# Kernel optimization log

Measured on AMD Instinct MI355X. Metric: run time of the kernel, lower is better.

## Reference

```python
import jax, jax.numpy as jnp
import numpy as np

WINDOW = 2048
STRIDE = 512
FREQ = WINDOW // 2  # 1024
FRAMES = 63
SIG_LEN = FRAMES * STRIDE  # 32256
BATCH = 64


def _make_kernels():
    # Hann window, sym=False: w[n] = 0.5*(1 - cos(2*pi*n/N))
    n = np.arange(WINDOW)
    window = 0.5 * (1.0 - np.cos(2.0 * np.pi * n / WINDOW))
    f = np.arange(FREQ)
    # basis[f, n] = exp(-2j*pi*f*n/N) * window[n]  (first N/2 rows of windowed DFT)
    phase = -2.0 * np.pi * np.outer(f, n) / WINDOW
    real = (np.cos(phase) * window[None, :]).T[:, None, :]  # [W, 1, F]
    imag = (np.sin(phase) * window[None, :]).T[:, None, :]  # [W, 1, F]
    return jnp.asarray(real, jnp.float32), jnp.asarray(imag, jnp.float32)


def setup_inputs() -> dict:
    key = jax.random.key(0)
    input_signal = jax.random.normal(key, (BATCH, SIG_LEN, 1), dtype=jnp.float32)
    real_kernel, imag_kernel = _make_kernels()
    return {"input_signal": input_signal, "real_kernel": real_kernel, "imag_kernel": imag_kernel}


def _stft(x, k):
    # TF 'same' padding for stride 512, kernel 2048, out = ceil(L/512) = 63:
    # total_pad = (out-1)*stride + kernel - L = 62*512 + 2048 - 32256 = 1536
    pad_l, pad_r = 768, 768
    return jax.lax.conv_general_dilated(
        x, k, window_strides=(STRIDE,), padding=[(pad_l, pad_r)],
        dimension_numbers=("NWC", "WIO", "NWC"))  # [B, 63, 1024]


def reference(input_signal, real_kernel, imag_kernel):
    real = _stft(input_signal, real_kernel)
    imag = _stft(input_signal, imag_kernel)
    real = real.reshape(-1, FRAMES, FREQ, 1)
    imag = imag.reshape(-1, FRAMES, FREQ, 1)
    return real, imag
```

## Files before the change

### kernel.cpp

```cpp
#include <hip/hip_runtime.h>
#include <hip/hip_bf16.h>

#define WINDOW   2048
#define STRIDE   512
#define FREQ     1024
#define FRAMES   63
#define SIG_LEN  32256
#define BATCH    64
#define PAD      768
#define XPAD_LEN 33792
#define M_TOTAL  4032
#define N_TOTAL  2048
#define K_TOTAL  2048

#define BM 128
#define BN 128
#define BK 64

typedef __attribute__((ext_vector_type(8))) short short8;
typedef __attribute__((ext_vector_type(4))) float floatx4;

__device__ __forceinline__ ushort f2bf(float f) {
    __hip_bfloat16 h = __float2bfloat16(f);
    return *reinterpret_cast<ushort*>(&h);
}

__global__ void pad_signal(const float4* __restrict__ x, uint4* __restrict__ xpad) {
    int id = blockIdx.x * blockDim.x + threadIdx.x;
    const int GP = XPAD_LEN / 8;
    if (id >= BATCH * GP) return;
    int b = id / GP, i = id - b * GP;
    ushort o[8] = {0, 0, 0, 0, 0, 0, 0, 0};
    int s = i - PAD / 8;
    if (s >= 0 && s < SIG_LEN / 8) {
        const float4* px = x + (size_t)b * (SIG_LEN / 4) + s * 2;
        float4 v0 = px[0], v1 = px[1];
        o[0] = f2bf(v0.x); o[1] = f2bf(v0.y); o[2] = f2bf(v0.z); o[3] = f2bf(v0.w);
        o[4] = f2bf(v1.x); o[5] = f2bf(v1.y); o[6] = f2bf(v1.z); o[7] = f2bf(v1.w);
    }
    xpad[id] = *(uint4*)o;
}

__global__ void build_bt(const float* __restrict__ kr,
                         const float* __restrict__ ki,
                         ushort* __restrict__ bt) {
    __shared__ __align__(16) ushort tile[64][72];
    const int tid = threadIdx.x;
    const int kt = blockIdx.x, nt = blockIdx.y;
    const int gn0 = nt * 64;
    const float* src = (gn0 < FREQ) ? kr : ki;
    const int n0 = gn0 - ((gn0 < FREQ) ? 0 : FREQ);
#pragma unroll
    for (int i = 0; i < 2; ++i) {
        int chunk = i * 256 + tid;
        int k = chunk >> 3, nc = chunk & 7;
        const float* p = src + (size_t)(kt * 64 + k) * FREQ + n0 + nc * 8;
        float4 v0 = *(const float4*)p;
        float4 v1 = *(const float4*)(p + 4);
        ushort tmp[8];
        tmp[0] = f2bf(v0.x); tmp[1] = f2bf(v0.y); tmp[2] = f2bf(v0.z); tmp[3] = f2bf(v0.w);
        tmp[4] = f2bf(v1.x); tmp[5] = f2bf(v1.y); tmp[6] = f2bf(v1.z); tmp[7] = f2bf(v1.w);
        *(uint4*)(&tile[k][nc * 8]) = *(uint4*)tmp;
    }
    __syncthreads();
#pragma unroll
    for (int i = 0; i < 2; ++i) {
        int chunk = i * 256 + tid;
        int n = chunk >> 3, kc = chunk & 7;
        ushort tmp[8];
#pragma unroll
        for (int j = 0; j < 8; ++j) tmp[j] = tile[kc * 8 + j][n];
        *(uint4*)(bt + (size_t)(gn0 + n) * K_TOTAL + kt * 64 + kc * 8) = *(uint4*)tmp;
    }
}

__device__ __forceinline__ void gload16(const ushort* g, ushort* l) {
    __builtin_amdgcn_global_load_lds(
        (const __attribute__((address_space(1))) unsigned int*)g,
        (__attribute__((address_space(3))) unsigned int*)l,
        16, 0, 0);
}

__global__ __launch_bounds__(256) void stft_gemm(
    const ushort* __restrict__ xpad, const ushort* __restrict__ bt,
    float* __restrict__ out) {
    __shared__ __align__(16) ushort As[2 * BM * 32];
    __shared__ __align__(16) ushort Bs[2 * BN * 32];

    const int tid  = threadIdx.x;
    const int lane = tid & 63;
    const int w    = tid >> 6;
    const int mtile = blockIdx.x;
    const int ntile = blockIdx.y;

    const int srow = w * 16 + (lane >> 2);
    const int kcol = ((lane & 3) ^ ((lane >> 3) & 3)) * 8;

    int gr0 = mtile * BM + srow;
    int gr1 = gr0 + 64;
    gr0 = min(gr0, M_TOTAL - 1);
    gr1 = min(gr1, M_TOTAL - 1);
    const int b0 = gr0 / FRAMES, t0 = gr0 - b0 * FRAMES;
    const int b1 = gr1 / FRAMES, t1 = gr1 - b1 * FRAMES;
    const ushort* gA0 = xpad + (size_t)b0 * XPAD_LEN + t0 * STRIDE + kcol;
    const ushort* gA1 = xpad + (size_t)b1 * XPAD_LEN + t1 * STRIDE + kcol;
    const ushort* gB0 = bt + (size_t)(ntile * BN + srow) * K_TOTAL + kcol;
    const ushort* gB1 = gB0 + (size_t)64 * K_TOTAL;

    ushort* ldsA0 = As + w * 512;
    ushort* ldsA1 = As + 2048 + w * 512;
    ushort* ldsB0 = Bs + w * 512;
    ushort* ldsB1 = Bs + 2048 + w * 512;

    const int wm = w >> 1, wn = w & 1;
    const int frow = lane & 15, fq = lane >> 4;
    const int cs = (fq ^ ((frow >> 1) & 3)) * 8;
    const ushort* pA = As + (wm * 64 + frow) * 32 + cs;
    const ushort* pB = Bs + (wn * 64 + frow) * 32 + cs;

    floatx4 acc[4][4];
#pragma unroll
    for (int mi = 0; mi < 4; ++mi)
#pragma unroll
        for (int ni = 0; ni < 4; ++ni)
            acc[mi][ni] = (floatx4){0.f, 0.f, 0.f, 0.f};

    for (int kt = 0; kt < K_TOTAL / BK; ++kt) {
        __syncthreads();
        gload16(gA0,      ldsA0);
        gload16(gA0 + 32, ldsA0 + 4096);
        gload16(gA1,      ldsA1);
        gload16(gA1 + 32, ldsA1 + 4096);
        gload16(gB0,      ldsB0);
        gload16(gB0 + 32, ldsB0 + 4096);
        gload16(gB1,      ldsB1);
        gload16(gB1 + 32, ldsB1 + 4096);
        gA0 += BK; gA1 += BK; gB0 += BK; gB1 += BK;
        __syncthreads();

#pragma unroll
        for (int kk = 0; kk < 2; ++kk) {
            short8 a[4], b[4];
#pragma unroll
            for (int mi = 0; mi < 4; ++mi)
                a[mi] = *(const short8*)(pA + kk * 4096 + mi * 512);
#pragma unroll
            for (int ni = 0; ni < 4; ++ni)
                b[ni] = *(const short8*)(pB + kk * 4096 + ni * 512);
#pragma unroll
            for (int mi = 0; mi < 4; ++mi)
#pragma unroll
                for (int ni = 0; ni < 4; ++ni)
                    acc[mi][ni] = __builtin_amdgcn_mfma_f32_16x16x32_bf16(
                        a[mi], b[ni], acc[mi][ni], 0, 0, 0);
        }
    }

    const int orow0 = mtile * BM + wm * 64 + fq * 4;
    const bool is_imag = (ntile >= 8);
    float* outp = out + (is_imag ? (size_t)M_TOTAL * FREQ : 0);
    const int ncol0 = (ntile - (is_imag ? 8 : 0)) * BN + wn * 64 + frow;

#pragma unroll
    for (int mi = 0; mi < 4; ++mi) {
#pragma unroll
        for (int r = 0; r < 4; ++r) {
            int grow = orow0 + mi * 16 + r;
            if (grow < M_TOTAL) {
                float* orow = outp + (size_t)grow * FREQ + ncol0;
#pragma unroll
                for (int ni = 0; ni < 4; ++ni)
                    orow[ni * 16] = acc[mi][ni][r];
            }
        }
    }
}

extern "C" void kernel_launch(void* const* d_in, const int* in_sizes, int n_in,
                              void* d_out, int out_size, void* d_ws, size_t ws_size,
                              hipStream_t stream) {
    const float* x  = (const float*)d_in[0];
    const float* kr = (const float*)d_in[1];
    const float* ki = (const float*)d_in[2];

    ushort* xpad = (ushort*)d_ws;
    ushort* btm  = xpad + (size_t)BATCH * XPAD_LEN;

    pad_signal<<<(BATCH * XPAD_LEN / 8 + 255) / 256, 256, 0, stream>>>(
        (const float4*)x, (uint4*)xpad);
    build_bt<<<dim3(K_TOTAL / 64, N_TOTAL / 64), 256, 0, stream>>>(kr, ki, btm);
    stft_gemm<<<dim3((M_TOTAL + BM - 1) / BM, N_TOTAL / BN), 256, 0, stream>>>(
        xpad, btm, (float*)d_out);
}
```

Measured before the change: 118.6 us.

## Register-prefetch next K tile instead of direct global-to-LDS loads

Replaces the global_load_lds direct copies with ordinary global loads into registers that are issued for the next K tile while the current tile's MFMAs run. The registers are then stored to LDS at the top of the next iteration. This is meant to hide global memory latency behind compute, since the previous loop waited on each load before computing. The cost is more VGPR pressure and extra LDS store instructions, and occupancy may drop as a result.

New measurement: 122.3 us. +3.1%, slower.

```diff
diff --git a/kernel.cpp b/kernel.cpp
--- a/kernel.cpp
+++ b/kernel.cpp
@@ -74,13 +74,6 @@
     }
 }
 
-__device__ __forceinline__ void gload16(const ushort* g, ushort* l) {
-    __builtin_amdgcn_global_load_lds(
-        (const __attribute__((address_space(1))) unsigned int*)g,
-        (__attribute__((address_space(3))) unsigned int*)l,
-        16, 0, 0);
-}
-
 __global__ __launch_bounds__(256) void stft_gemm(
     const ushort* __restrict__ xpad, const ushort* __restrict__ bt,
     float* __restrict__ out) {
@@ -107,10 +100,14 @@
     const ushort* gB0 = bt + (size_t)(ntile * BN + srow) * K_TOTAL + kcol;
     const ushort* gB1 = gB0 + (size_t)64 * K_TOTAL;
 
-    ushort* ldsA0 = As + w * 512;
-    ushort* ldsA1 = As + 2048 + w * 512;
-    ushort* ldsB0 = Bs + w * 512;
-    ushort* ldsB1 = Bs + 2048 + w * 512;
+    uint4* sA0 = (uint4*)(As + w * 512) + lane;
+    uint4* sA0h = (uint4*)(As + w * 512 + 4096) + lane;
+    uint4* sA1 = (uint4*)(As + 2048 + w * 512) + lane;
+    uint4* sA1h = (uint4*)(As + 2048 + w * 512 + 4096) + lane;
+    uint4* sB0 = (uint4*)(Bs + w * 512) + lane;
+    uint4* sB0h = (uint4*)(Bs + w * 512 + 4096) + lane;
+    uint4* sB1 = (uint4*)(Bs + 2048 + w * 512) + lane;
+    uint4* sB1h = (uint4*)(Bs + 2048 + w * 512 + 4096) + lane;
 
     const int wm = w >> 1, wn = w & 1;
     const int frow = lane & 15, fq = lane >> 4;
@@ -125,35 +122,52 @@
         for (int ni = 0; ni < 4; ++ni)
             acc[mi][ni] = (floatx4){0.f, 0.f, 0.f, 0.f};
 
+    uint4 va0, va0h, va1, va1h, vb0, vb0h, vb1, vb1h;
+    va0  = *(const uint4*)gA0;  va0h = *(const uint4*)(gA0 + 32);
+    va1  = *(const uint4*)gA1;  va1h = *(const uint4*)(gA1 + 32);
+    vb0  = *(const uint4*)gB0;  vb0h = *(const uint4*)(gB0 + 32);
+    vb1  = *(const uint4*)gB1;  vb1h = *(const uint4*)(gB1 + 32);
+    gA0 += BK; gA1 += BK; gB0 += BK; gB1 += BK;
+
     for (int kt = 0; kt < K_TOTAL / BK; ++kt) {
         __syncthreads();
-        gload16(gA0,      ldsA0);
-        gload16(gA0 + 32, ldsA0 + 4096);
-        gload16(gA1,      ldsA1);
-        gload16(gA1 + 32, ldsA1 + 4096);
-        gload16(gB0,      ldsB0);
-        gload16(gB0 + 32, ldsB0 + 4096);
-        gload16(gB1,      ldsB1);
-        gload16(gB1 + 32, ldsB1 + 4096);
-        gA0 += BK; gA1 += BK; gB0 += BK; gB1 += BK;
+        *sA0 = va0;  *sA0h = va0h;
+        *sA1 = va1;  *sA1h = va1h;
+        *sB0 = vb0;  *sB0h = vb0h;
+        *sB1 = vb1;  *sB1h = vb1h;
         __syncthreads();
 
-#pragma unroll
-        for (int kk = 0; kk < 2; ++kk) {
-            short8 a[4], b[4];
-#pragma unroll
-            for (int mi = 0; mi < 4; ++mi)
-                a[mi] = *(const short8*)(pA + kk * 4096 + mi * 512);
+        short8 a[4], b[4];
+#pragma unroll
+        for (int mi = 0; mi < 4; ++mi) a[mi] = *(const short8*)(pA + mi * 512);
+#pragma unroll
+        for (int ni = 0; ni < 4; ++ni) b[ni] = *(const short8*)(pB + ni * 512);
+
+        if (kt < K_TOTAL / BK - 1) {
+            va0  = *(const uint4*)gA0;  va0h = *(const uint4*)(gA0 + 32);
+            va1  = *(const uint4*)gA1;  va1h = *(const uint4*)(gA1 + 32);
+            vb0  = *(const uint4*)gB0;  vb0h = *(const uint4*)(gB0 + 32);
+            vb1  = *(const uint4*)gB1;  vb1h = *(const uint4*)(gB1 + 32);
+            gA0 += BK; gA1 += BK; gB0 += BK; gB1 += BK;
+        }
+
+#pragma unroll
+        for (int mi = 0; mi < 4; ++mi)
 #pragma unroll
             for (int ni = 0; ni < 4; ++ni)
-                b[ni] = *(const short8*)(pB + kk * 4096 + ni * 512);
-#pragma unroll
-            for (int mi = 0; mi < 4; ++mi)
-#pragma unroll
-                for (int ni = 0; ni < 4; ++ni)
-                    acc[mi][ni] = __builtin_amdgcn_mfma_f32_16x16x32_bf16(
-                        a[mi], b[ni], acc[mi][ni], 0, 0, 0);
-        }
+                acc[mi][ni] = __builtin_amdgcn_mfma_f32_16x16x32_bf16(
+                    a[mi], b[ni], acc[mi][ni], 0, 0, 0);
+
+#pragma unroll
+        for (int mi = 0; mi < 4; ++mi) a[mi] = *(const short8*)(pA + 4096 + mi * 512);
+#pragma unroll
+        for (int ni = 0; ni < 4; ++ni) b[ni] = *(const short8*)(pB + 4096 + ni * 512);
+#pragma unroll
+        for (int mi = 0; mi < 4; ++mi)
+#pragma unroll
+            for (int ni = 0; ni < 4; ++ni)
+                acc[mi][ni] = __builtin_amdgcn_mfma_f32_16x16x32_bf16(
+                    a[mi], b[ni], acc[mi][ni], 0, 0, 0);
     }
 
     const int orow0 = mtile * BM + wm * 64 + fq * 4;
```

## Switch GEMM to 32x32x16 MFMA and fuse the prep kernels into one launch

Applied to the files above, without the earlier changes.

The GEMM inner loop now uses 32x32x16 bf16 MFMA tiles, two by two per wave, in place of sixteen 16x16x32 tiles, with new LDS addressing and output index mapping. This cuts LDS fragment reads per MFMA and the number of MFMA issues. Separately, the pad and basis-transpose kernels are merged into one launch, with a block-index split, to save one kernel launch. The new swizzle and lane mapping must line up with the existing store layout or results will be wrong.

New measurement: 116.0 us. -2.2%, faster.

```diff
diff --git a/kernel.cpp b/kernel.cpp
--- a/kernel.cpp
+++ b/kernel.cpp
@@ -17,60 +17,63 @@
 #define BN 128
 #define BK 64
 
-typedef __attribute__((ext_vector_type(8))) short short8;
-typedef __attribute__((ext_vector_type(4))) float floatx4;
+#define PAD_BLOCKS 1056
+
+typedef __attribute__((ext_vector_type(8)))  short short8;
+typedef __attribute__((ext_vector_type(16))) float floatx16;
 
 __device__ __forceinline__ ushort f2bf(float f) {
     __hip_bfloat16 h = __float2bfloat16(f);
     return *reinterpret_cast<ushort*>(&h);
 }
 
-__global__ void pad_signal(const float4* __restrict__ x, uint4* __restrict__ xpad) {
-    int id = blockIdx.x * blockDim.x + threadIdx.x;
-    const int GP = XPAD_LEN / 8;
-    if (id >= BATCH * GP) return;
-    int b = id / GP, i = id - b * GP;
-    ushort o[8] = {0, 0, 0, 0, 0, 0, 0, 0};
-    int s = i - PAD / 8;
-    if (s >= 0 && s < SIG_LEN / 8) {
-        const float4* px = x + (size_t)b * (SIG_LEN / 4) + s * 2;
-        float4 v0 = px[0], v1 = px[1];
-        o[0] = f2bf(v0.x); o[1] = f2bf(v0.y); o[2] = f2bf(v0.z); o[3] = f2bf(v0.w);
-        o[4] = f2bf(v1.x); o[5] = f2bf(v1.y); o[6] = f2bf(v1.z); o[7] = f2bf(v1.w);
-    }
-    xpad[id] = *(uint4*)o;
-}
-
-__global__ void build_bt(const float* __restrict__ kr,
-                         const float* __restrict__ ki,
-                         ushort* __restrict__ bt) {
-    __shared__ __align__(16) ushort tile[64][72];
+__global__ __launch_bounds__(256) void prep_fused(
+    const float* __restrict__ x, const float* __restrict__ kr,
+    const float* __restrict__ ki, ushort* __restrict__ xpad_o,
+    ushort* __restrict__ bt) {
     const int tid = threadIdx.x;
-    const int kt = blockIdx.x, nt = blockIdx.y;
-    const int gn0 = nt * 64;
-    const float* src = (gn0 < FREQ) ? kr : ki;
-    const int n0 = gn0 - ((gn0 < FREQ) ? 0 : FREQ);
+    if (blockIdx.x < PAD_BLOCKS) {
+        int id = blockIdx.x * 256 + tid;
+        const int GP = XPAD_LEN / 8;
+        int b = id / GP, i = id - b * GP;
+        ushort o[8] = {0, 0, 0, 0, 0, 0, 0, 0};
+        int s = i - PAD / 8;
+        if (s >= 0 && s < SIG_LEN / 8) {
+            const float4* px = (const float4*)x + (size_t)b * (SIG_LEN / 4) + s * 2;
+            float4 v0 = px[0], v1 = px[1];
+            o[0] = f2bf(v0.x); o[1] = f2bf(v0.y); o[2] = f2bf(v0.z); o[3] = f2bf(v0.w);
+            o[4] = f2bf(v1.x); o[5] = f2bf(v1.y); o[6] = f2bf(v1.z); o[7] = f2bf(v1.w);
+        }
+        ((uint4*)xpad_o)[id] = *(uint4*)o;
+    } else {
+        __shared__ __align__(16) ushort tile[64][72];
+        const int bid = blockIdx.x - PAD_BLOCKS;
+        const int kt = bid & 31, nt = bid >> 5;
+        const int gn0 = nt * 64;
+        const float* src = (gn0 < FREQ) ? kr : ki;
+        const int n0 = gn0 - ((gn0 < FREQ) ? 0 : FREQ);
 #pragma unroll
-    for (int i = 0; i < 2; ++i) {
-        int chunk = i * 256 + tid;
-        int k = chunk >> 3, nc = chunk & 7;
-        const float* p = src + (size_t)(kt * 64 + k) * FREQ + n0 + nc * 8;
-        float4 v0 = *(const float4*)p;
-        float4 v1 = *(const float4*)(p + 4);
-        ushort tmp[8];
-        tmp[0] = f2bf(v0.x); tmp[1] = f2bf(v0.y); tmp[2] = f2bf(v0.z); tmp[3] = f2bf(v0.w);
-        tmp[4] = f2bf(v1.x); tmp[5] = f2bf(v1.y); tmp[6] = f2bf(v1.z); tmp[7] = f2bf(v1.w);
-        *(uint4*)(&tile[k][nc * 8]) = *(uint4*)tmp;
-    }
-    __syncthreads();
+        for (int i = 0; i < 2; ++i) {
+            int chunk = i * 256 + tid;
+            int k = chunk >> 3, nc = chunk & 7;
+            const float* p = src + (size_t)(kt * 64 + k) * FREQ + n0 + nc * 8;
+            float4 v0 = *(const float4*)p;
+            float4 v1 = *(const float4*)(p + 4);
+            ushort tmp[8];
+            tmp[0] = f2bf(v0.x); tmp[1] = f2bf(v0.y); tmp[2] = f2bf(v0.z); tmp[3] = f2bf(v0.w);
+            tmp[4] = f2bf(v1.x); tmp[5] = f2bf(v1.y); tmp[6] = f2bf(v1.z); tmp[7] = f2bf(v1.w);
+            *(uint4*)(&tile[k][nc * 8]) = *(uint4*)tmp;
+        }
+        __syncthreads();
 #pragma unroll
-    for (int i = 0; i < 2; ++i) {
-        int chunk = i * 256 + tid;
-        int n = chunk >> 3, kc = chunk & 7;
-        ushort tmp[8];
+        for (int i = 0; i < 2; ++i) {
+            int chunk = i * 256 + tid;
+            int n = chunk >> 3, kc = chunk & 7;
+            ushort tmp[8];
 #pragma unroll
-        for (int j = 0; j < 8; ++j) tmp[j] = tile[kc * 8 + j][n];
-        *(uint4*)(bt + (size_t)(gn0 + n) * K_TOTAL + kt * 64 + kc * 8) = *(uint4*)tmp;
+            for (int j = 0; j < 8; ++j) tmp[j] = tile[kc * 8 + j][n];
+            *(uint4*)(bt + (size_t)(gn0 + n) * K_TOTAL + kt * 64 + kc * 8) = *(uint4*)tmp;
+        }
     }
 }
 
@@ -113,17 +116,19 @@
     ushort* ldsB1 = Bs + 2048 + w * 512;
 
     const int wm = w >> 1, wn = w & 1;
-    const int frow = lane & 15, fq = lane >> 4;
-    const int cs = (fq ^ ((frow >> 1) & 3)) * 8;
-    const ushort* pA = As + (wm * 64 + frow) * 32 + cs;
-    const ushort* pB = Bs + (wn * 64 + frow) * 32 + cs;
+    const int fr32 = lane & 31;
+    const int kg   = lane >> 5;
+    const int rsw = (fr32 >> 1) & 3;
+    const ushort* pA = As + (wm * 64 + fr32) * 32;
+    const ushort* pB = Bs + (wn * 64 + fr32) * 32;
 
-    floatx4 acc[4][4];
+    floatx16 acc[2][2];
 #pragma unroll
-    for (int mi = 0; mi < 4; ++mi)
+    for (int mi = 0; mi < 2; ++mi)
 #pragma unroll
-        for (int ni = 0; ni < 4; ++ni)
-            acc[mi][ni] = (floatx4){0.f, 0.f, 0.f, 0.f};
+        for (int ni = 0; ni < 2; ++ni)
+#pragma unroll
+            for (int r = 0; r < 16; ++r) acc[mi][ni][r] = 0.f;
 
     for (int kt = 0; kt < K_TOTAL / BK; ++kt) {
         __syncthreads();
@@ -139,38 +144,39 @@
         __syncthreads();
 
 #pragma unroll
-        for (int kk = 0; kk < 2; ++kk) {
-            short8 a[4], b[4];
+        for (int s = 0; s < 4; ++s) {
+            const int off = (s >> 1) * 4096 + (((s & 1) * 2 + kg) ^ rsw) * 8;
+            short8 a[2], b[2];
 #pragma unroll
-            for (int mi = 0; mi < 4; ++mi)
-                a[mi] = *(const short8*)(pA + kk * 4096 + mi * 512);
+            for (int mi = 0; mi < 2; ++mi)
+                a[mi] = *(const short8*)(pA + mi * 32 * 32 + off);
 #pragma unroll
-            for (int ni = 0; ni < 4; ++ni)
-                b[ni] = *(const short8*)(pB + kk * 4096 + ni * 512);
+            for (int ni = 0; ni < 2; ++ni)
+                b[ni] = *(const short8*)(pB + ni * 32 * 32 + off);
 #pragma unroll
-            for (int mi = 0; mi < 4; ++mi)
+            for (int mi = 0; mi < 2; ++mi)
 #pragma unroll
-                for (int ni = 0; ni < 4; ++ni)
-                    acc[mi][ni] = __builtin_amdgcn_mfma_f32_16x16x32_bf16(
+                for (int ni = 0; ni < 2; ++ni)
+                    acc[mi][ni] = __builtin_amdgcn_mfma_f32_32x32x16_bf16(
                         a[mi], b[ni], acc[mi][ni], 0, 0, 0);
         }
     }
 
-    const int orow0 = mtile * BM + wm * 64 + fq * 4;
+    const int orow_base = mtile * BM + wm * 64;
     const bool is_imag = (ntile >= 8);
     float* outp = out + (is_imag ? (size_t)M_TOTAL * FREQ : 0);
-    const int ncol0 = (ntile - (is_imag ? 8 : 0)) * BN + wn * 64 + frow;
+    const int ncol_base = (ntile - (is_imag ? 8 : 0)) * BN + wn * 64 + fr32;
 
 #pragma unroll
-    for (int mi = 0; mi < 4; ++mi) {
+    for (int mi = 0; mi < 2; ++mi) {
 #pragma unroll
-        for (int r = 0; r < 4; ++r) {
-            int grow = orow0 + mi * 16 + r;
+        for (int r = 0; r < 16; ++r) {
+            int grow = orow_base + mi * 32 + (r & 3) + 8 * (r >> 2) + 4 * kg;
             if (grow < M_TOTAL) {
-                float* orow = outp + (size_t)grow * FREQ + ncol0;
+                float* orow = outp + (size_t)grow * FREQ + ncol_base;
 #pragma unroll
-                for (int ni = 0; ni < 4; ++ni)
-                    orow[ni * 16] = acc[mi][ni][r];
+                for (int ni = 0; ni < 2; ++ni)
+                    orow[ni * 32] = acc[mi][ni][r];
             }
         }
     }
@@ -186,9 +192,7 @@
     ushort* xpad = (ushort*)d_ws;
     ushort* btm  = xpad + (size_t)BATCH * XPAD_LEN;
 
-    pad_signal<<<(BATCH * XPAD_LEN / 8 + 255) / 256, 256, 0, stream>>>(
-        (const float4*)x, (uint4*)xpad);
-    build_bt<<<dim3(K_TOTAL / 64, N_TOTAL / 64), 256, 0, stream>>>(kr, ki, btm);
+    prep_fused<<<PAD_BLOCKS + 1024, 256, 0, stream>>>(x, kr, ki, xpad, btm);
     stft_gemm<<<dim3((M_TOTAL + BM - 1) / BM, N_TOTAL / BN), 256, 0, stream>>>(
         xpad, btm, (float*)d_out);
 }
```
